# Kernel optimization log

Measured on AMD Instinct MI355X. Metric: run time of the kernel, lower is better.

## Reference

```python
import jax, jax.numpy as jnp
import numpy as np

N_NODES = 16384
K_NBR = 16
N_HOPS = 4  # hops + 2
IN_DIM = 256
RAW_DIM = 128
OUT_DIM = 64
PHI_DIM = 16
N_KERN = 4
E = N_NODES * K_NBR


def setup_inputs() -> dict:
    key = jax.random.key(0)
    ks = jax.random.split(key, 16)
    s = 0.05  # small weight scale for numerical sanity
    h = jax.random.normal(ks[0], (N_NODES, IN_DIM), jnp.float32)
    e_tensor = jax.random.normal(ks[1], (N_HOPS, N_NODES, RAW_DIM), jnp.float32)
    # kNN-style edges: each dst node has exactly K_NBR incoming edges
    src = jax.random.randint(ks[2], (N_HOPS, E), 0, N_NODES, jnp.int32)
    dst = jnp.tile(jnp.repeat(jnp.arange(N_NODES, dtype=jnp.int32), K_NBR)[None, :], (N_HOPS, 1))
    return {
        'h': h,
        'e_tensor': e_tensor,
        'src': src,
        'dst': dst,
        'W_phi': jax.random.normal(ks[3], (N_HOPS, RAW_DIM, PHI_DIM - 1), jnp.float32) * s,
        'mlp_w1': jax.random.normal(ks[4], (N_HOPS, RAW_DIM, IN_DIM), jnp.float32) * s,
        'mlp_b1': jax.random.normal(ks[5], (N_HOPS, IN_DIM), jnp.float32) * s,
        'mlp_w2': jax.random.normal(ks[6], (N_HOPS, IN_DIM, PHI_DIM * N_KERN), jnp.float32) * s,
        'mlp_b2': jax.random.normal(ks[7], (N_HOPS, PHI_DIM * N_KERN), jnp.float32) * s,
        'tilde_phi': jax.random.normal(ks[8], (N_HOPS, N_KERN, PHI_DIM), jnp.float32),
        'W': jax.random.normal(ks[9], (N_HOPS, IN_DIM, OUT_DIM * N_KERN), jnp.float32) * s,
        'bias': jax.random.normal(ks[10], (N_HOPS, OUT_DIM), jnp.float32) * s,
        'z': jax.random.normal(ks[11], (OUT_DIM, 1), jnp.float32),
    }


def _deform_gconv(h, e_l, src, dst, W_phi, w1, b1, w2, b2, tilde_phi, W, bias):
    N = h.shape[0]
    nk, phi_dim = tilde_phi.shape
    hk = (h @ W).reshape(N, nk, -1)                                  # (N, nk, out)
    phi = e_l @ W_phi                                                # (N, phi-1)
    tn = tilde_phi / jnp.linalg.norm(tilde_phi, axis=1, keepdims=True)  # (nk, phi)
    hid = jax.nn.relu(e_l @ w1 + b1)
    delta = (hid @ w2 + b2).reshape(N, nk, phi_dim)                  # (N, nk, phi)
    delta_ik = tn[None, :, :] + delta                                # (N, nk, phi)
    # per-edge quantities (edges carry dst-node delta_ik, u_sub_v distance)
    dist = phi[src] - phi[dst]                                       # (E, phi-1)
    last = jnp.all(dist == 0, axis=1, keepdims=True).astype(dist.dtype)
    dist = jnp.concatenate([dist, last], axis=1)                     # (E, phi)
    dist = dist / jnp.maximum(jnp.linalg.norm(dist, axis=1, keepdims=True), 1e-8)
    logits = jnp.einsum('ep,ekp->ek', dist, delta_ik[dst])           # (E, nk)
    # edge_softmax over incoming edges of each dst node
    mx = jax.ops.segment_max(logits, dst, num_segments=N)
    ex = jnp.exp(logits - mx[dst])
    den = jax.ops.segment_sum(ex, dst, num_segments=N)
    att = ex / den[dst]                                              # (E, nk)
    # message passing: m = h[src] * att, sum over incoming edges
    m = hk[src] * att[:, :, None]                                    # (E, nk, out)
    agg = jax.ops.segment_sum(m, dst, num_segments=N)                # (N, nk, out)
    out = agg.sum(1) + bias[None, :]
    out = out / jnp.maximum(jnp.linalg.norm(out, axis=1, keepdims=True), 1e-8)
    # regularizers
    d = tn[:, None, :] - tn[None, :, :]                              # (nk, nk, phi)
    l_sep = jnp.sum(jnp.sum(d * d, axis=-1)) / nk                    # sum_i mean_j ||t_i - t_j||^2
    l_focus = jnp.mean(jnp.sum(delta * delta, axis=2))
    return out, l_sep, l_focus


def reference(h, e_tensor, src, dst, W_phi, mlp_w1, mlp_b1, mlp_w2, mlp_b2, tilde_phi, W, bias, z):
    outs, l_seps, l_fos = jax.vmap(
        _deform_gconv, in_axes=(None, 0, 0, 0, 0, 0, 0, 0, 0, 0, 0, 0)
    )(h, e_tensor, src, dst, W_phi, mlp_w1, mlp_b1, mlp_w2, mlp_b2, tilde_phi, W, bias)
    # hop-level softmax fusion
    score = jnp.einsum('hno,oz->hnz', outs, z)                       # (n_hops, N, 1)
    att = jax.nn.softmax(score, axis=0)
    tilde_h = jnp.sum(att * outs, axis=0)                            # (N, out)
    l_sep = jnp.mean(l_seps)
    l_focus = jnp.mean(l_fos)
    return tilde_h, l_sep, l_focus
```

## Files before the change

### kernel.cpp

```cpp
#include <hip/hip_runtime.h>
#include <hip/hip_bf16.h>

#define N_NODES 16384
#define K_NBR 16
#define HOPS 4
#define IN_DIM 256
#define RAW_DIM 128
#define OUT_DIM 64
#define PHI_DIM 16
#define N_KERN 4
#define E_EDGES (N_NODES * K_NBR)

typedef __hip_bfloat16 bf16;
typedef __attribute__((ext_vector_type(8))) short short8;
typedef __attribute__((ext_vector_type(4))) float f32x4;
typedef __attribute__((ext_vector_type(4))) unsigned int uint4v;

__device__ __forceinline__ float toF(float x) { return x; }
__device__ __forceinline__ float toF(bf16 x) { return __bfloat162float(x); }
__device__ __forceinline__ short f2bfbits(float f)
{
    bf16 b = __float2bfloat16(f);
    short s; __builtin_memcpy(&s, &b, 2); return s;
}

#define CV_WPHI 0
#define CV_W1   (CV_WPHI + HOPS * RAW_DIM * (PHI_DIM - 1))
#define CV_B1   (CV_W1 + HOPS * RAW_DIM * IN_DIM)
#define CV_W2   (CV_B1 + HOPS * IN_DIM)
#define CV_B2   (CV_W2 + HOPS * IN_DIM * PHI_DIM * N_KERN)
#define CV_TPHI (CV_B2 + HOPS * PHI_DIM * N_KERN)
#define CV_W    (CV_TPHI + HOPS * N_KERN * PHI_DIM)
#define CV_BIAS (CV_W + HOPS * IN_DIM * OUT_DIM * N_KERN)
#define CV_Z    (CV_BIAS + HOPS * OUT_DIM)
#define CV_END  (CV_Z + OUT_DIM)

#define WT_N  (HOPS * 256 * 256)
#define W1T_N (HOPS * 256 * 128)
#define W2T_N (HOPS * 64 * 256)
#define WPT_N (HOPS * 16 * 128)
#define CVT_TOTAL (WT_N + W1T_N + W2T_N + WPT_N)

#define NB_CV ((CV_END + 255) / 256)
#define NB_WT (CVT_TOTAL / 256)
#define NB_H  (N_NODES * 256 / 8 / 256)
#define NB_E  (HOPS * N_NODES * 128 / 8 / 256)
#define NB_ALL (NB_CV + NB_WT + NB_H + NB_E + 1)

__device__ __forceinline__ float loadDyn(const void* p, int i, bool isbf)
{
    return isbf ? toF(((const bf16*)p)[i]) : ((const float*)p)[i];
}

__device__ __forceinline__ void cvt8(bf16* dst, const void* src, size_t base, bool isbf)
{
    short8 v;
    if (isbf) {
        v = *(const short8*)((const bf16*)src + base);
    } else {
        const float* sp = (const float*)src + base;
        f32x4 f0 = *(const f32x4*)sp;
        f32x4 f1 = *(const f32x4*)(sp + 4);
#pragma unroll
        for (int j = 0; j < 4; j++) { v[j] = f2bfbits(f0[j]); v[4 + j] = f2bfbits(f1[j]); }
    }
    *(short8*)(dst + base) = v;
}

__global__ __launch_bounds__(256) void cvt_all(
    const void* h, const void* e,
    const void* wphi, const void* w1, const void* b1, const void* w2,
    const void* b2, const void* tphi, const void* W, const void* bias,
    const void* z, float* __restrict__ CV,
    bf16* __restrict__ wt, bf16* __restrict__ w1t, bf16* __restrict__ w2t,
    bf16* __restrict__ wpt, bf16* __restrict__ h_bf, bf16* __restrict__ e_bf,
    float* __restrict__ tn_out, float* __restrict__ acc, int* __restrict__ flagOut)
{
    __shared__ float s_det[4];
    int tid = threadIdx.x;
    {
        unsigned short pv = ((const unsigned short*)h)[tid];
        unsigned int bits = ((unsigned int)pv) << 16;
        float v; __builtin_memcpy(&v, &bits, 4);
        v = fabsf(v);
        if (!(v == v) || v > 1e30f) v = 1e30f;
#pragma unroll
        for (int off = 32; off > 0; off >>= 1) v = fmaxf(v, __shfl_xor(v, off));
        if ((tid & 63) == 0) s_det[tid >> 6] = v;
    }
    __syncthreads();
    bool isbf = fmaxf(fmaxf(s_det[0], s_det[1]), fmaxf(s_det[2], s_det[3])) < 1e4f;

    int b = blockIdx.x;
    if (b == NB_ALL - 1) {
        __shared__ float s_v[256], s_tn[256], s_red[256], s_hop[4];
        int hop = tid >> 6, t64 = tid & 63;
        int row = t64 >> 4, p = t64 & 15;
        float v = loadDyn(tphi, hop * 64 + t64, isbf);
        s_v[tid] = v;
        __syncthreads();
        float ss = 0.f;
        for (int q = 0; q < 16; q++) { float x = s_v[hop * 64 + row * 16 + q]; ss += x * x; }
        float tnv = v / sqrtf(ss);
        tn_out[hop * 64 + t64] = tnv;
        s_tn[tid] = tnv;
        __syncthreads();
        float s = 0.f;
        for (int j = 0; j < 4; j++) {
            float d = tnv - s_tn[hop * 64 + j * 16 + p];
            s += d * d;
        }
        s_red[tid] = s;
        __syncthreads();
        if (t64 == 0) {
            float tot = 0.f;
            for (int i = 0; i < 64; i++) tot += s_red[hop * 64 + i];
            s_hop[hop] = tot;
        }
        __syncthreads();
        if (tid == 0) {
            acc[0] = (s_hop[0] + s_hop[1] + s_hop[2] + s_hop[3]) * 0.0625f;
            acc[1] = 0.f;
            *flagOut = isbf ? 1 : 0;
        }
        return;
    }
    if (b < NB_CV) {
        int idx = b * 256 + tid;
        if (idx >= CV_END) return;
        float v;
        if      (idx < CV_W1)   v = loadDyn(wphi, idx - CV_WPHI, isbf);
        else if (idx < CV_B1)   v = loadDyn(w1,   idx - CV_W1,   isbf);
        else if (idx < CV_W2)   v = loadDyn(b1,   idx - CV_B1,   isbf);
        else if (idx < CV_B2)   v = loadDyn(w2,   idx - CV_W2,   isbf);
        else if (idx < CV_TPHI) v = loadDyn(b2,   idx - CV_B2,   isbf);
        else if (idx < CV_W)    v = loadDyn(tphi, idx - CV_TPHI, isbf);
        else if (idx < CV_BIAS) v = loadDyn(W,    idx - CV_W,    isbf);
        else if (idx < CV_Z)    v = loadDyn(bias, idx - CV_BIAS, isbf);
        else                    v = loadDyn(z,    idx - CV_Z,    isbf);
        CV[idx] = v;
        return;
    }
    b -= NB_CV;
    if (b < NB_WT) {
        int idx = b * 256 + tid;
        if (idx < WT_N) {
            int o = idx, hop = o >> 16, rem = o & 65535, n = rem >> 8, k = rem & 255;
            wt[o] = __float2bfloat16(loadDyn(W, hop * 65536 + k * 256 + n, isbf));
        } else if (idx < WT_N + W1T_N) {
            int o = idx - WT_N, hop = o >> 15, rem = o & 32767, n = rem >> 7, k = rem & 127;
            w1t[o] = __float2bfloat16(loadDyn(w1, hop * 32768 + k * 256 + n, isbf));
        } else if (idx < WT_N + W1T_N + W2T_N) {
            int o = idx - WT_N - W1T_N, hop = o >> 14, rem = o & 16383, n = rem >> 8, k = rem & 255;
            w2t[o] = __float2bfloat16(loadDyn(w2, hop * 16384 + k * 64 + n, isbf));
        } else {
            int o = idx - WT_N - W1T_N - W2T_N, hop = o >> 11, rem = o & 2047, n = rem >> 7, k = rem & 127;
            float v = (n < 15) ? loadDyn(wphi, hop * 1920 + k * 15 + n, isbf) : 0.f;
            wpt[o] = __float2bfloat16(v);
        }
        return;
    }
    b -= NB_WT;
    if (b < NB_H) {
        size_t base = ((size_t)b * 256 + tid) * 8;
        cvt8(h_bf, h, base, isbf);
        return;
    }
    b -= NB_H;
    {
        size_t base = ((size_t)b * 256 + tid) * 8;
        cvt8(e_bf, e, base, isbf);
    }
}

template <int BN, int WR, int WC, int OUTMODE, bool STAGED>
__device__ __forceinline__ void gemm_dev(
    char* smem, const bf16* __restrict__ A, const bf16* __restrict__ Bt,
    void* __restrict__ Cg, int K, int N, int colBase)
{
    constexpr int WM = 128 / WR;
    constexpr int WN = BN / WC;
    constexpr int MT = WM / 16;
    constexpr int NT = WN / 16;
    constexpr int ESZ = (OUTMODE == 0) ? 4 : 1;
    short* As = (short*)smem;
    short* Bs = As + 128 * 72;

    int tid = threadIdx.x;
    int w = tid >> 6, lane = tid & 63;
    int wr = w / WC, wc = w % WC;
    int l16 = lane & 15, quad = lane >> 4;
    int rowBase = blockIdx.y * 128;

    f32x4 acc[MT][NT] = {};

    for (int k0 = 0; k0 < K; k0 += 64) {
        for (int c = tid; c < 128 * 8; c += 256) {
            int row = c >> 3, c8 = c & 7;
            *(short8*)&As[row * 72 + c8 * 8] =
                *(const short8*)(A + (size_t)(rowBase + row) * K + k0 + c8 * 8);
        }
        for (int c = tid; c < BN * 8; c += 256) {
            int row = c >> 3, c8 = c & 7;
            *(short8*)&Bs[row * 72 + c8 * 8] =
                *(const short8*)(Bt + (size_t)(colBase + row) * K + k0 + c8 * 8);
        }
        __syncthreads();
#pragma unroll
        for (int kc = 0; kc < 64; kc += 32) {
            short8 aF[MT], bF[NT];
#pragma unroll
            for (int mi = 0; mi < MT; mi++)
                aF[mi] = *(const short8*)&As[(wr * WM + mi * 16 + l16) * 72 + kc + quad * 8];
#pragma unroll
            for (int ni = 0; ni < NT; ni++)
                bF[ni] = *(const short8*)&Bs[(wc * WN + ni * 16 + l16) * 72 + kc + quad * 8];
#pragma unroll
            for (int mi = 0; mi < MT; mi++)
#pragma unroll
                for (int ni = 0; ni < NT; ni++)
                    acc[mi][ni] = __builtin_amdgcn_mfma_f32_16x16x32_bf16(
                        aF[mi], bF[ni], acc[mi][ni], 0, 0, 0);
        }
        __syncthreads();
    }

#pragma unroll
    for (int mi = 0; mi < MT; mi++) {
#pragma unroll
        for (int ni = 0; ni < NT; ni++) {
            int cl = wc * WN + ni * 16 + l16;
            int col = colBase + cl;
#pragma unroll
            for (int r = 0; r < 4; r++) {
                int rl = wr * WM + mi * 16 + quad * 4 + r;
                float v = acc[mi][ni][r];
                if (STAGED) {
                    size_t idx = (size_t)rl * BN + cl;
                    if (OUTMODE == 0) ((float*)smem)[idx] = v;
                    else {
                        int pk = __builtin_amdgcn_cvt_pk_fp8_f32(v, v, 0, false);
                        ((unsigned char*)smem)[idx] = (unsigned char)(pk & 0xFF);
                    }
                } else {
                    ((float*)Cg)[(size_t)(rowBase + rl) * N + col] = v;
                }
            }
        }
    }
    if (STAGED) {
        __syncthreads();
        constexpr int CPR = BN * ESZ / 16;
        for (int c = tid; c < 128 * CPR; c += 256) {
            int r = c / CPR, off = (c % CPR) * 16;
            *(uint4v*)((char*)Cg + ((size_t)(rowBase + r) * N + colBase) * ESZ + off) =
                *(const uint4v*)(smem + (size_t)r * BN * ESZ + off);
        }
    }
}

__global__ __launch_bounds__(256) void hkphi_kernel(
    const bf16* __restrict__ h_bf, const bf16* __restrict__ e_bf,
    const bf16* __restrict__ WT, const bf16* __restrict__ WPT,
    unsigned char* __restrict__ hk_f8, float* __restrict__ phi)
{
    __shared__ __align__(16) char smem[128 * 72 * 2 + 128 * 72 * 2];
    int hop = blockIdx.z;
    if (blockIdx.x < 2) {
        gemm_dev<128, 2, 2, 2, true>(
            smem, h_bf, WT + (size_t)hop * 256 * 256,
            hk_f8 + (size_t)hop * N_NODES * 256, 256, 256, blockIdx.x * 128);
    } else {
        gemm_dev<16, 4, 1, 0, false>(
            smem, e_bf + (size_t)hop * N_NODES * 128, WPT + (size_t)hop * 16 * 128,
            phi + (size_t)hop * N_NODES * 16, 128, 16, 0);
    }
}

__global__ __launch_bounds__(256) void hid_delta_kernel(
    const bf16* __restrict__ e_bf, const bf16* __restrict__ W1T,
    const bf16* __restrict__ W2T, const float* __restrict__ b1All,
    const float* __restrict__ b2All, const float* __restrict__ tnAll,
    float* __restrict__ DELTA, float* __restrict__ lfocus)
{
    __shared__ __align__(16) char smem[64 * 72 * 2 + 256 * 72 * 2 + 64 * 264 * 2];
    __shared__ float s_w[4];
    short* As  = (short*)smem;
    short* Bs  = As + 64 * 72;
    short* Hs  = Bs + 256 * 72;
    short* B2s = Bs;
    float* Ds  = (float*)smem;

    int hop = blockIdx.y;
    int rowBase = blockIdx.x * 64;
    const bf16* A  = e_bf + (size_t)hop * N_NODES * 128;
    const bf16* B1 = W1T + (size_t)hop * 256 * 128;
    const bf16* B2 = W2T + (size_t)hop * 64 * 256;
    const float* b1 = b1All + hop * 256;
    const float* b2 = b2All + hop * 64;
    const float* tn = tnAll + hop * 64;

    int tid = threadIdx.x;
    int w = tid >> 6, lane = tid & 63;
    int l16 = lane & 15, quad = lane >> 4;

    {
        f32x4 acc[4][4] = {};
        for (int k0 = 0; k0 < 128; k0 += 64) {
            for (int c = tid; c < 64 * 8; c += 256) {
                int row = c >> 3, c8 = c & 7;
                *(short8*)&As[row * 72 + c8 * 8] =
                    *(const short8*)(A + (size_t)(rowBase + row) * 128 + k0 + c8 * 8);
            }
            for (int c = tid; c < 256 * 8; c += 256) {
                int row = c >> 3, c8 = c & 7;
                *(short8*)&Bs[row * 72 + c8 * 8] =
                    *(const short8*)(B1 + (size_t)row * 128 + k0 + c8 * 8);
            }
            __syncthreads();
#pragma unroll
            for (int kc = 0; kc < 64; kc += 32) {
                short8 aF[4], bF[4];
#pragma unroll
                for (int mi = 0; mi < 4; mi++)
                    aF[mi] = *(const short8*)&As[(mi * 16 + l16) * 72 + kc + quad * 8];
#pragma unroll
                for (int ni = 0; ni < 4; ni++)
                    bF[ni] = *(const short8*)&Bs[(w * 64 + ni * 16 + l16) * 72 + kc + quad * 8];
#pragma unroll
                for (int mi = 0; mi < 4; mi++)
#pragma unroll
                    for (int ni = 0; ni < 4; ni++)
                        acc[mi][ni] = __builtin_amdgcn_mfma_f32_16x16x32_bf16(
                            aF[mi], bF[ni], acc[mi][ni], 0, 0, 0);
            }
            __syncthreads();
        }
#pragma unroll
        for (int mi = 0; mi < 4; mi++) {
#pragma unroll
            for (int ni = 0; ni < 4; ni++) {
                int col = w * 64 + ni * 16 + l16;
                float bv = b1[col];
#pragma unroll
                for (int r = 0; r < 4; r++) {
                    int row = mi * 16 + quad * 4 + r;
                    float v = fmaxf(acc[mi][ni][r] + bv, 0.f);
                    Hs[row * 264 + col] = f2bfbits(v);
                }
            }
        }
        for (int c = tid; c < 64 * 32; c += 256) {
            int row = c >> 5, ch = c & 31;
            *(short8*)&B2s[row * 264 + ch * 8] =
                *(const short8*)(B2 + (size_t)row * 256 + ch * 8);
        }
        __syncthreads();
    }

    {
        f32x4 acc2[4] = {};
        for (int kc = 0; kc < 256; kc += 32) {
            short8 aF = *(const short8*)&Hs[(w * 16 + l16) * 264 + kc + quad * 8];
            short8 bF[4];
#pragma unroll
            for (int ni = 0; ni < 4; ni++)
                bF[ni] = *(const short8*)&B2s[(ni * 16 + l16) * 264 + kc + quad * 8];
#pragma unroll
            for (int ni = 0; ni < 4; ni++)
                acc2[ni] = __builtin_amdgcn_mfma_f32_16x16x32_bf16(aF, bF[ni], acc2[ni], 0, 0, 0);
        }
        __syncthreads();
        float sq = 0.f;
#pragma unroll
        for (int ni = 0; ni < 4; ni++) {
            int col = ni * 16 + l16;
            float bv = b2[col], tv = tn[col];
#pragma unroll
            for (int r = 0; r < 4; r++) {
                int row = w * 16 + quad * 4 + r;
                float v = acc2[ni][r] + bv;
                sq += v * v;
                Ds[row * 64 + col] = v + tv;
            }
        }
#pragma unroll
        for (int off = 32; off > 0; off >>= 1) sq += __shfl_xor(sq, off);
        if (lane == 0) s_w[w] = sq;
        __syncthreads();
        float* Dg = DELTA + (size_t)hop * N_NODES * 64;
        for (int c = tid; c < 64 * 16; c += 256) {
            int r = c >> 4, off = (c & 15) * 4;
            *(uint4v*)(Dg + (size_t)(rowBase + r) * 64 + off) =
                *(const uint4v*)(Ds + (size_t)r * 64 + off);
        }
        if (tid == 0) atomicAdd(lfocus, s_w[0] + s_w[1] + s_w[2] + s_w[3]);
    }
}

__global__ __launch_bounds__(256) void edge_agg2(
    const unsigned char* __restrict__ hk, const float* __restrict__ phi,
    const float* __restrict__ dik, const int* __restrict__ src,
    const float* __restrict__ biasAll, float* __restrict__ outs)
{
    int b = blockIdx.x;
    int hop = b & 3;
    int wave = threadIdx.x >> 6, lane = threadIdx.x & 63;
    int node = (b >> 2) * 4 + wave;
    const unsigned char* hk_l = hk + (size_t)hop * N_NODES * 256;
    const float* phi_l  = phi + (size_t)hop * N_NODES * 16;
    const float* dik_l  = dik + (size_t)hop * N_NODES * 64;
    const int*   src_n  = src + (size_t)hop * E_EDGES + (size_t)node * 16;
    const float* bias_l = biasAll + hop * 64;
    float*       outs_n = outs + ((size_t)hop * N_NODES + node) * 64;

    __shared__ float s_dik[4][64];
    __shared__ __align__(16) float s_attT[4][4][24];
    __shared__ int   s_src[4][16];

    s_dik[wave][lane] = dik_l[(size_t)node * 64 + lane];
    if (lane < 16) s_src[wave][lane] = src_n[lane];

    int e = lane >> 2, q = lane & 3;
    int sN = s_src[wave][e];
    f32x4 ps = *(const f32x4*)(phi_l + (size_t)sN * 16 + q * 4);
    f32x4 pd = *(const f32x4*)(phi_l + (size_t)node * 16 + q * 4);
    float d0 = ps[0] - pd[0], d1 = ps[1] - pd[1];
    float d2 = ps[2] - pd[2], d3 = ps[3] - pd[3];
    bool q3 = (q == 3);
    float nzf = ((d0 != 0.f) | (d1 != 0.f) | (d2 != 0.f) | (!q3 && d3 != 0.f)) ? 1.f : 0.f;
    float ssp = d0 * d0 + d1 * d1 + d2 * d2 + (q3 ? 0.f : d3 * d3);
    nzf += __shfl_xor(nzf, 1); nzf += __shfl_xor(nzf, 2);
    ssp += __shfl_xor(ssp, 1); ssp += __shfl_xor(ssp, 2);
    float last = (nzf == 0.f) ? 1.f : 0.f;
    if (q3) d3 = last;
    float inv = 1.f / fmaxf(sqrtf(ssp + last * last), 1e-8f);
#pragma unroll
    for (int k = 0; k < 4; k++) {
        const float* dk = &s_dik[wave][k * 16 + q * 4];
        float pk = d0 * dk[0] + d1 * dk[1] + d2 * dk[2] + d3 * dk[3];
        pk += __shfl_xor(pk, 1); pk += __shfl_xor(pk, 2);
        if (q == k) s_attT[wave][k][e] = pk * inv;
    }

    int k2 = lane & 3;
    float lgv = s_attT[wave][k2][e];
    float mx = lgv;
    mx = fmaxf(mx, __shfl_xor(mx, 4));
    mx = fmaxf(mx, __shfl_xor(mx, 8));
    mx = fmaxf(mx, __shfl_xor(mx, 16));
    mx = fmaxf(mx, __shfl_xor(mx, 32));
    float ex = __expf(lgv - mx);
    float den = ex;
    den += __shfl_xor(den, 4);
    den += __shfl_xor(den, 8);
    den += __shfl_xor(den, 16);
    den += __shfl_xor(den, 32);
    s_attT[wave][k2][e] = ex / den;

    int kk = lane >> 4, dsub = (lane & 15) * 4;
    f32x4 attv[4];
#pragma unroll
    for (int g = 0; g < 4; g++) attv[g] = *(const f32x4*)&s_attT[wave][kk][g * 4];
    float a0 = 0.f, a1 = 0.f, a2 = 0.f, a3 = 0.f;
#pragma unroll
    for (int ee = 0; ee < 16; ee++) {
        int sm = __builtin_amdgcn_readfirstlane(s_src[wave][ee]);
        unsigned int u = *(const unsigned int*)(hk_l + (size_t)sm * 256 + lane * 4);
        float wgt = attv[ee >> 2][ee & 3];
        auto lo = __builtin_amdgcn_cvt_pk_f32_fp8((int)u, false);
        auto hi = __builtin_amdgcn_cvt_pk_f32_fp8((int)u, true);
        a0 += wgt * lo[0];
        a1 += wgt * lo[1];
        a2 += wgt * hi[0];
        a3 += wgt * hi[1];
    }
    a0 += __shfl_xor(a0, 16); a0 += __shfl_xor(a0, 32);
    a1 += __shfl_xor(a1, 16); a1 += __shfl_xor(a1, 32);
    a2 += __shfl_xor(a2, 16); a2 += __shfl_xor(a2, 32);
    a3 += __shfl_xor(a3, 16); a3 += __shfl_xor(a3, 32);
    float o0 = a0 + bias_l[dsub + 0];
    float o1 = a1 + bias_l[dsub + 1];
    float o2 = a2 + bias_l[dsub + 2];
    float o3 = a3 + bias_l[dsub + 3];
    float ssq = o0 * o0 + o1 * o1 + o2 * o2 + o3 * o3;
    ssq += __shfl_xor(ssq, 1);
    ssq += __shfl_xor(ssq, 2);
    ssq += __shfl_xor(ssq, 4);
    ssq += __shfl_xor(ssq, 8);
    float inv2 = 1.f / fmaxf(sqrtf(ssq), 1e-8f);
    if (kk == 0) {
        f32x4 st;
        st[0] = o0 * inv2; st[1] = o1 * inv2; st[2] = o2 * inv2; st[3] = o3 * inv2;
        *(f32x4*)(outs_n + dsub) = st;
    }
}

__global__ __launch_bounds__(256) void fuse_kernel(
    const float* __restrict__ outs, const float* __restrict__ z,
    void* __restrict__ out, const int* __restrict__ flag,
    const float* __restrict__ acc)
{
    int tid = threadIdx.x;
    int node = blockIdx.x * 4 + (tid >> 6);
    int dd = tid & 63;
    float zv = z[dd];
    float o[4], sc[4];
#pragma unroll
    for (int h = 0; h < 4; h++) {
        o[h] = outs[((size_t)h * N_NODES + node) * 64 + dd];
        float v = o[h] * zv;
#pragma unroll
        for (int off = 32; off > 0; off >>= 1) v += __shfl_xor(v, off);
        sc[h] = v;
    }
    float mx = fmaxf(fmaxf(sc[0], sc[1]), fmaxf(sc[2], sc[3]));
    float e0 = __expf(sc[0] - mx), e1 = __expf(sc[1] - mx);
    float e2 = __expf(sc[2] - mx), e3 = __expf(sc[3] - mx);
    float den = e0 + e1 + e2 + e3;
    float t = (e0 * o[0] + e1 * o[1] + e2 * o[2] + e3 * o[3]) / den;
    size_t oi = (size_t)node * 64 + dd;
    bool isbf = (*flag != 0);
    if (isbf) ((bf16*)out)[oi] = __float2bfloat16(t);
    else      ((float*)out)[oi] = t;
    if (blockIdx.x == 0 && tid == 0) {
        float a = acc[0];
        float b = acc[1] / ((float)N_NODES * 4.f * 4.f);
        size_t base = (size_t)N_NODES * 64;
        if (isbf) {
            ((bf16*)out)[base]     = __float2bfloat16(a);
            ((bf16*)out)[base + 1] = __float2bfloat16(b);
        } else {
            ((float*)out)[base]     = a;
            ((float*)out)[base + 1] = b;
        }
    }
}

extern "C" void kernel_launch(void* const* d_in, const int* in_sizes, int n_in,
                              void* d_out, int out_size, void* d_ws, size_t ws_size,
                              hipStream_t stream)
{
    const void* h    = d_in[0];
    const void* e    = d_in[1];
    const int*  src  = (const int*)d_in[2];
    const void* Wphi = d_in[4];
    const void* w1   = d_in[5];
    const void* b1   = d_in[6];
    const void* w2   = d_in[7];
    const void* b2   = d_in[8];
    const void* tphi = d_in[9];
    const void* W    = d_in[10];
    const void* bias = d_in[11];
    const void* z    = d_in[12];

    float* ws    = (float*)d_ws;
    float* CV    = ws;
    float* OUTS  = CV + CV_END;
    float* PHI   = OUTS + (size_t)4 * N_NODES * 64;
    float* DELTA = PHI + (size_t)4 * N_NODES * 16;
    float* TN    = DELTA + (size_t)4 * N_NODES * 64;
    float* ACC   = TN + 256;
    int*   FLAG  = (int*)(ACC + 2);
    bf16*  H_BF  = (bf16*)(ACC + 4);
    bf16*  E_BF  = H_BF + (size_t)N_NODES * 256;
    bf16*  WT    = E_BF + (size_t)HOPS * N_NODES * 128;
    bf16*  W1T   = WT + WT_N;
    bf16*  W2T   = W1T + W1T_N;
    bf16*  WPT   = W2T + W2T_N;
    unsigned char* HK_F8 = (unsigned char*)(WPT + WPT_N);

    cvt_all<<<NB_ALL, 256, 0, stream>>>(
        h, e, Wphi, w1, b1, w2, b2, tphi, W, bias, z, CV,
        WT, W1T, W2T, WPT, H_BF, E_BF, TN, ACC, FLAG);

    hkphi_kernel<<<dim3(3, 128, HOPS), 256, 0, stream>>>(
        H_BF, E_BF, WT, WPT, HK_F8, PHI);
    hid_delta_kernel<<<dim3(N_NODES / 64, HOPS), 256, 0, stream>>>(
        E_BF, W1T, W2T, CV + CV_B1, CV + CV_B2, TN, DELTA, ACC + 1);
    edge_agg2<<<dim3(N_NODES), 256, 0, stream>>>(
        HK_F8, PHI, DELTA, src, CV + CV_BIAS, OUTS);

    fuse_kernel<<<dim3(N_NODES / 4), 256, 0, stream>>>(
        OUTS, CV + CV_Z, d_out, FLAG, ACC);
}
```

Baseline: 232.6 us.

## Merge hk/phi and hid/delta GEMM kernels into one interleaved launch

Combines the hk/phi GEMM kernel and the hidden-MLP/delta kernel into a single launch of 2560 blocks. Block indices interleave the two kinds of work so the GPU stays busy and one kernel boundary disappears. In exchange the merged kernel uses the larger shared-memory footprint for every block, which can lower occupancy for the GEMM blocks. Two small edits ride along: the zero-distance check now reuses the squared-norm sum, and the bias is read with one vector load.

```diff
diff --git a/kernel.cpp b/kernel.cpp
--- a/kernel.cpp
+++ b/kernel.cpp
@@ -46,6 +46,10 @@
 #define NB_H  (N_NODES * 256 / 8 / 256)
 #define NB_E  (HOPS * N_NODES * 128 / 8 / 256)
 #define NB_ALL (NB_CV + NB_WT + NB_H + NB_E + 1)
+
+#define GA_NA 1536
+#define GA_NB 1024
+#define GA_TOTAL (GA_NA + GA_NB)
 
 __device__ __forceinline__ float loadDyn(const void* p, int i, bool isbf)
 {
@@ -176,7 +180,7 @@
 template <int BN, int WR, int WC, int OUTMODE, bool STAGED>
 __device__ __forceinline__ void gemm_dev(
     char* smem, const bf16* __restrict__ A, const bf16* __restrict__ Bt,
-    void* __restrict__ Cg, int K, int N, int colBase)
+    void* __restrict__ Cg, int K, int N, int colBase, int rowBase)
 {
     constexpr int WM = 128 / WR;
     constexpr int WN = BN / WC;
@@ -190,7 +194,6 @@
     int w = tid >> 6, lane = tid & 63;
     int wr = w / WC, wc = w % WC;
     int l16 = lane & 15, quad = lane >> 4;
-    int rowBase = blockIdx.y * 128;
 
     f32x4 acc[MT][NT] = {};
 
@@ -259,46 +262,18 @@
     }
 }
 
-__global__ __launch_bounds__(256) void hkphi_kernel(
-    const bf16* __restrict__ h_bf, const bf16* __restrict__ e_bf,
-    const bf16* __restrict__ WT, const bf16* __restrict__ WPT,
-    unsigned char* __restrict__ hk_f8, float* __restrict__ phi)
-{
-    __shared__ __align__(16) char smem[128 * 72 * 2 + 128 * 72 * 2];
-    int hop = blockIdx.z;
-    if (blockIdx.x < 2) {
-        gemm_dev<128, 2, 2, 2, true>(
-            smem, h_bf, WT + (size_t)hop * 256 * 256,
-            hk_f8 + (size_t)hop * N_NODES * 256, 256, 256, blockIdx.x * 128);
-    } else {
-        gemm_dev<16, 4, 1, 0, false>(
-            smem, e_bf + (size_t)hop * N_NODES * 128, WPT + (size_t)hop * 16 * 128,
-            phi + (size_t)hop * N_NODES * 16, 128, 16, 0);
-    }
-}
-
-__global__ __launch_bounds__(256) void hid_delta_kernel(
-    const bf16* __restrict__ e_bf, const bf16* __restrict__ W1T,
-    const bf16* __restrict__ W2T, const float* __restrict__ b1All,
-    const float* __restrict__ b2All, const float* __restrict__ tnAll,
-    float* __restrict__ DELTA, float* __restrict__ lfocus)
-{
-    __shared__ __align__(16) char smem[64 * 72 * 2 + 256 * 72 * 2 + 64 * 264 * 2];
-    __shared__ float s_w[4];
+__device__ __forceinline__ void hid_delta_dev(
+    char* smem, float* s_w,
+    const bf16* __restrict__ A, const bf16* __restrict__ B1,
+    const bf16* __restrict__ B2, const float* __restrict__ b1,
+    const float* __restrict__ b2, const float* __restrict__ tn,
+    float* __restrict__ Dg, float* __restrict__ lfocus, int rowBase)
+{
     short* As  = (short*)smem;
     short* Bs  = As + 64 * 72;
     short* Hs  = Bs + 256 * 72;
     short* B2s = Bs;
     float* Ds  = (float*)smem;
-
-    int hop = blockIdx.y;
-    int rowBase = blockIdx.x * 64;
-    const bf16* A  = e_bf + (size_t)hop * N_NODES * 128;
-    const bf16* B1 = W1T + (size_t)hop * 256 * 128;
-    const bf16* B2 = W2T + (size_t)hop * 64 * 256;
-    const float* b1 = b1All + hop * 256;
-    const float* b2 = b2All + hop * 64;
-    const float* tn = tnAll + hop * 64;
 
     int tid = threadIdx.x;
     int w = tid >> 6, lane = tid & 63;
@@ -388,13 +363,48 @@
         for (int off = 32; off > 0; off >>= 1) sq += __shfl_xor(sq, off);
         if (lane == 0) s_w[w] = sq;
         __syncthreads();
-        float* Dg = DELTA + (size_t)hop * N_NODES * 64;
         for (int c = tid; c < 64 * 16; c += 256) {
             int r = c >> 4, off = (c & 15) * 4;
             *(uint4v*)(Dg + (size_t)(rowBase + r) * 64 + off) =
                 *(const uint4v*)(Ds + (size_t)r * 64 + off);
         }
         if (tid == 0) atomicAdd(lfocus, s_w[0] + s_w[1] + s_w[2] + s_w[3]);
+    }
+}
+
+__global__ __launch_bounds__(256) void gemm_all(
+    const bf16* __restrict__ h_bf, const bf16* __restrict__ e_bf,
+    const bf16* __restrict__ WT, const bf16* __restrict__ WPT,
+    const bf16* __restrict__ W1T, const bf16* __restrict__ W2T,
+    const float* __restrict__ b1All, const float* __restrict__ b2All,
+    const float* __restrict__ tnAll, unsigned char* __restrict__ hk_f8,
+    float* __restrict__ phi, float* __restrict__ DELTA, float* __restrict__ lfocus)
+{
+    __shared__ __align__(16) char smem[64 * 72 * 2 + 256 * 72 * 2 + 64 * 264 * 2];
+    __shared__ float s_w[4];
+    int b = blockIdx.x;
+    bool isA;
+    int a;
+    if (b < 2 * GA_NB) { isA = !(b & 1); a = b >> 1; }
+    else               { isA = true;     a = GA_NB + (b - 2 * GA_NB); }
+    if (isA) {
+        int hop = a / 384, r = a % 384, part = r >> 7, row = r & 127;
+        if (part < 2) {
+            gemm_dev<128, 2, 2, 2, true>(
+                smem, h_bf, WT + (size_t)hop * 256 * 256,
+                hk_f8 + (size_t)hop * N_NODES * 256, 256, 256, part * 128, row * 128);
+        } else {
+            gemm_dev<16, 4, 1, 0, false>(
+                smem, e_bf + (size_t)hop * N_NODES * 128, WPT + (size_t)hop * 16 * 128,
+                phi + (size_t)hop * N_NODES * 16, 128, 16, 0, row * 128);
+        }
+    } else {
+        int hop = a >> 8, tile = a & 255;
+        hid_delta_dev(smem, s_w,
+            e_bf + (size_t)hop * N_NODES * 128,
+            W1T + (size_t)hop * 256 * 128, W2T + (size_t)hop * 64 * 256,
+            b1All + hop * 256, b2All + hop * 64, tnAll + hop * 64,
+            DELTA + (size_t)hop * N_NODES * 64, lfocus, tile * 64);
     }
 }
 
@@ -428,11 +438,9 @@
     float d0 = ps[0] - pd[0], d1 = ps[1] - pd[1];
     float d2 = ps[2] - pd[2], d3 = ps[3] - pd[3];
     bool q3 = (q == 3);
-    float nzf = ((d0 != 0.f) | (d1 != 0.f) | (d2 != 0.f) | (!q3 && d3 != 0.f)) ? 1.f : 0.f;
     float ssp = d0 * d0 + d1 * d1 + d2 * d2 + (q3 ? 0.f : d3 * d3);
-    nzf += __shfl_xor(nzf, 1); nzf += __shfl_xor(nzf, 2);
     ssp += __shfl_xor(ssp, 1); ssp += __shfl_xor(ssp, 2);
-    float last = (nzf == 0.f) ? 1.f : 0.f;
+    float last = (ssp == 0.f) ? 1.f : 0.f;
     if (q3) d3 = last;
     float inv = 1.f / fmaxf(sqrtf(ssp + last * last), 1e-8f);
 #pragma unroll
@@ -479,10 +487,11 @@
     a1 += __shfl_xor(a1, 16); a1 += __shfl_xor(a1, 32);
     a2 += __shfl_xor(a2, 16); a2 += __shfl_xor(a2, 32);
     a3 += __shfl_xor(a3, 16); a3 += __shfl_xor(a3, 32);
-    float o0 = a0 + bias_l[dsub + 0];
-    float o1 = a1 + bias_l[dsub + 1];
-    float o2 = a2 + bias_l[dsub + 2];
-    float o3 = a3 + bias_l[dsub + 3];
+    f32x4 bv = *(const f32x4*)(bias_l + dsub);
+    float o0 = a0 + bv[0];
+    float o1 = a1 + bv[1];
+    float o2 = a2 + bv[2];
+    float o3 = a3 + bv[3];
     float ssq = o0 * o0 + o1 * o1 + o2 * o2 + o3 * o3;
     ssq += __shfl_xor(ssq, 1);
     ssq += __shfl_xor(ssq, 2);
@@ -574,10 +583,10 @@
         h, e, Wphi, w1, b1, w2, b2, tphi, W, bias, z, CV,
         WT, W1T, W2T, WPT, H_BF, E_BF, TN, ACC, FLAG);
 
-    hkphi_kernel<<<dim3(3, 128, HOPS), 256, 0, stream>>>(
-        H_BF, E_BF, WT, WPT, HK_F8, PHI);
-    hid_delta_kernel<<<dim3(N_NODES / 64, HOPS), 256, 0, stream>>>(
-        E_BF, W1T, W2T, CV + CV_B1, CV + CV_B2, TN, DELTA, ACC + 1);
+    gemm_all<<<dim3(GA_TOTAL), 256, 0, stream>>>(
+        H_BF, E_BF, WT, WPT, W1T, W2T,
+        CV + CV_B1, CV + CV_B2, TN, HK_F8, PHI, DELTA, ACC + 1);
+
     edge_agg2<<<dim3(N_NODES), 256, 0, stream>>>(
         HK_F8, PHI, DELTA, src, CV + CV_BIAS, OUTS);
 
```

Result: faster. 215.2 us (-7.5%).
